# Optimization experiments

Measured on AMD Instinct MI355X. Metric: run time of the kernel, lower is better.

Reference implementation:

```python
import jax, jax.numpy as jnp
import numpy as np

TIMESTEPS = 1000

def _cosine_schedule(T, s=0.008):
    # Nichol & Dhariwal cosine schedule
    x = np.linspace(0.0, T, T + 1, dtype=np.float64)
    acp = np.cos(((x / T) + s) / (1.0 + s) * np.pi / 2.0) ** 2
    acp = acp / acp[0]
    betas = np.clip(1.0 - acp[1:] / acp[:-1], 1e-4, 0.999)
    alphas_cumprod = np.cumprod(1.0 - betas)
    return (betas.astype(np.float32),
            np.sqrt(alphas_cumprod).astype(np.float32),
            np.sqrt(1.0 - alphas_cumprod).astype(np.float32))

BETAS, SQRT_ACP, SQRT_OM_ACP = _cosine_schedule(TIMESTEPS)

B = 2048            # crystals
N_PER = 64          # atoms per crystal (uniform ragged groups)
N = B * N_PER       # total atoms
NODE_DIM = 64
N_SPECIES = 100

def setup_inputs() -> dict:
    key = jax.random.key(0)
    ks = jax.random.split(key, 10)
    frac_coords = jax.random.uniform(ks[0], (N, 3), dtype=jnp.float32)
    noise = jax.random.normal(ks[1], (N, 3), dtype=jnp.float32)
    pred_noise = jax.random.normal(ks[2], (N, 3), dtype=jnp.float32)
    h_final = jax.random.normal(ks[3], (N, NODE_DIM), dtype=jnp.float32)
    # lattice: identity-dominated cells ~5 Angstrom with small perturbation
    lattice = 5.0 * jnp.eye(3, dtype=jnp.float32)[None] + 0.2 * jax.random.normal(ks[4], (B, 3, 3), dtype=jnp.float32)
    W1 = jax.random.normal(ks[5], (NODE_DIM, 128), dtype=jnp.float32) * (1.0 / np.sqrt(NODE_DIM))
    b1 = jnp.zeros((128,), dtype=jnp.float32)
    W2 = jax.random.normal(ks[6], (128, N_SPECIES), dtype=jnp.float32) * (1.0 / np.sqrt(128.0))
    b2 = jnp.zeros((N_SPECIES,), dtype=jnp.float32)
    t = jax.random.randint(ks[7], (B,), 0, TIMESTEPS)
    batch_indices = jnp.repeat(jnp.arange(B), N_PER)
    species = jax.random.randint(ks[8], (N,), 0, N_SPECIES)
    return {"frac_coords": frac_coords, "noise": noise, "pred_noise": pred_noise,
            "h_final": h_final, "lattice": lattice, "W1": W1, "b1": b1,
            "W2": W2, "b2": b2, "t": t, "batch_indices": batch_indices,
            "species": species}

def reference(frac_coords, noise, pred_noise, h_final, lattice, W1, b1, W2, b2,
              t, batch_indices, species):
    sqrt_acp = jnp.asarray(SQRT_ACP)
    sqrt_om = jnp.asarray(SQRT_OM_ACP)
    t_nodes = t[batch_indices]                       # [N]
    sa = sqrt_acp[t_nodes][:, None]                  # [N,1]
    so = sqrt_om[t_nodes][:, None]                   # [N,1]
    # q_sample + periodic wrap
    x_t = sa * frac_coords + so * noise
    x_t = x_t - jnp.floor(x_t)
    # diffusion MSE (dynamics output pred_noise supplied as input)
    loss_diffusion = jnp.mean((pred_noise - noise) ** 2)
    # predicted x0, wrapped
    pred_x0 = (x_t - so * pred_noise) / sa
    pred_x0 = pred_x0 - jnp.floor(pred_x0)
    # vectorized ragged PBC repulsion (uniform groups of N_PER atoms)
    bsz = lattice.shape[0]
    n = frac_coords.shape[0] // bsz
    f = pred_x0.reshape(bsz, n, 3)                   # [B,n,3]
    diff = f[:, :, None, :] - f[:, None, :, :]       # [B,n,n,3]
    diff = diff - jnp.round(diff)                    # minimum-image convention
    diff_c = jnp.einsum('bijk,bkl->bijl', diff, lattice)
    dist_sq = jnp.sum(diff_c ** 2, axis=-1)          # [B,n,n]
    eye = jnp.eye(n, dtype=bool)
    dist_sq = jnp.where(eye[None], 1e10, dist_sq)    # fill_diagonal_(inf)
    dist = jnp.sqrt(dist_sq + 1e-8)
    rep = jax.nn.relu(0.8 - dist) ** 2
    l_repulsion = jnp.sum(rep) / n / bsz
    loss_diffusion = loss_diffusion + 5.0 * l_repulsion
    # species head: Linear -> SiLU -> Linear, cross entropy
    hidden = jax.nn.silu(h_final @ W1 + b1)
    logits = hidden @ W2 + b2                        # [N,100]
    logp = jax.nn.log_softmax(logits, axis=-1)
    loss_species = -jnp.mean(jnp.take_along_axis(logp, species[:, None], axis=-1))
    return (loss_diffusion, loss_species, l_repulsion)
```

## Files before the change

kernel.cpp:

```cpp
#include <hip/hip_runtime.h>
#include <math.h>

#define TSTEPS   1000
#define NB       2048
#define NB2      1024
#define NPER     64
#define NATOMS   (NB*NPER)
#define NDIM     64
#define NHID     128
#define NSPEC    100

typedef __attribute__((ext_vector_type(8))) short bf16x8;
typedef __attribute__((ext_vector_type(4))) float f32x4;

__device__ inline short f2bf(float x) {
  unsigned u = __builtin_bit_cast(unsigned, x);
  u += 0x7fffu + ((u >> 16) & 1u);
  return (short)(u >> 16);
}

__global__ __launch_bounds__(256) void k_sched(float* __restrict__ sacp,
                                               float* __restrict__ som,
                                               const float* __restrict__ W1,
                                               const float* __restrict__ W2,
                                               const float* __restrict__ b2,
                                               unsigned short* __restrict__ w1f,
                                               unsigned short* __restrict__ w2f,
                                               float* __restrict__ b2p) {
  const int tid = threadIdx.x, blk = blockIdx.x;
  if (blk == 0) {
    if (tid < 112) b2p[tid] = (tid < NSPEC) ? b2[tid] : 0.0f;
    __shared__ double sh[256];
    const double PI = 3.14159265358979323846, s = 0.008;
    const int t0 = tid * 4;
    double lg[4], loc = 0.0;
    if (t0 < TSTEPS) {
      double c[5];
      #pragma unroll
      for (int i = 0; i < 5; ++i) {
        double u = (((double)(t0 + i) / (double)TSTEPS) + s) / (1.0 + s) * PI * 0.5;
        c[i] = cos(u);
      }
      #pragma unroll
      for (int i = 0; i < 4; ++i) {
        double beta = 1.0 - (c[i+1]*c[i+1]) / (c[i]*c[i]);
        beta = fmin(fmax(beta, 1e-4), 0.999);
        lg[i] = log(1.0 - beta);
        loc += lg[i];
      }
    }
    sh[tid] = loc;
    __syncthreads();
    for (int off = 1; off < 256; off <<= 1) {
      double add = (tid >= off) ? sh[tid - off] : 0.0;
      __syncthreads();
      sh[tid] += add;
      __syncthreads();
    }
    if (t0 < TSTEPS) {
      double run = sh[tid] - loc;
      #pragma unroll
      for (int i = 0; i < 4; ++i) {
        run += lg[i];
        double cum = exp(run);
        sacp[t0+i] = (float)sqrt(cum);
        som[t0+i]  = (float)sqrt(1.0 - cum);
      }
    }
  } else if (blk <= 4) {
    const int c0 = (blk - 1) * 256 + tid;
    const int lane = c0 & 63, t = c0 >> 6;
    const int kk = t & 1, nt = t >> 1;
    const int q = lane >> 4, l15 = lane & 15;
    __attribute__((aligned(16))) unsigned short v[8];
    #pragma unroll
    for (int j = 0; j < 8; ++j) {
      int k = kk*32 + q*8 + j;
      v[j] = (unsigned short)f2bf(W1[k*NHID + nt*16 + l15]);
    }
    *(uint4*)(w1f + (size_t)c0*8) = *(const uint4*)v;
  } else {
    for (int c0 = (blk - 5) * 256 + tid; c0 < 3584; c0 += 1792) {
      const int lane = c0 & 63, t = c0 >> 6;
      const int kk = t & 3, nt = t >> 2;
      const int q = lane >> 4, l15 = lane & 15;
      const int cls = nt*16 + l15;
      __attribute__((aligned(16))) unsigned short v[8];
      #pragma unroll
      for (int j = 0; j < 8; ++j) {
        int k = kk*32 + q*8 + j;
        v[j] = (cls < NSPEC) ? (unsigned short)f2bf(W2[k*NSPEC + cls]) : 0;
      }
      *(uint4*)(w2f + (size_t)c0*8) = *(const uint4*)v;
    }
  }
}

__global__ __launch_bounds__(256) void k_main(const float* __restrict__ hfin,
                                              const float* __restrict__ b1,
                                              const float* __restrict__ b2p,
                                              const int*   __restrict__ spec,
                                              const unsigned short* __restrict__ w1f,
                                              const unsigned short* __restrict__ w2f,
                                              const float* __restrict__ frac,
                                              const float* __restrict__ noise,
                                              const float* __restrict__ pnoise,
                                              const float* __restrict__ lattice,
                                              const int*   __restrict__ tarr,
                                              const float* __restrict__ sacp,
                                              const float* __restrict__ som,
                                              float* __restrict__ mseP,
                                              float* __restrict__ repP,
                                              float* __restrict__ specP) {
  __shared__ __attribute__((aligned(16))) unsigned short Hs[4*4096];
  const int tid  = threadIdx.x;
  const int wave = tid >> 6, lane = tid & 63;
  const int q = lane >> 4, l15 = lane & 15;
  const int b = blockIdx.x;
  const int atomBase = b * 128;
  unsigned short* HsW = Hs + wave*4096;

  const int cu = __builtin_amdgcn_readfirstlane(2*b + (wave >> 1));
  const int tt = tarr[cu];
  const float sa = sacp[tt], so = som[tt];
  const float rsa = __builtin_amdgcn_rcpf(sa);
  float px0, px1, px2, msep;
  {
    const size_t a = (size_t)cu*64 + lane;
    const float3 fr = *(const float3*)(frac   + 3*a);
    const float3 nz = *(const float3*)(noise  + 3*a);
    const float3 pn = *(const float3*)(pnoise + 3*a);
    float xt0 = fmaf(so, nz.x, sa*fr.x); xt0 -= floorf(xt0);
    float xt1 = fmaf(so, nz.y, sa*fr.y); xt1 -= floorf(xt1);
    float xt2 = fmaf(so, nz.z, sa*fr.z); xt2 -= floorf(xt2);
    px0 = (xt0 - so*pn.x)*rsa; px0 -= floorf(px0);
    px1 = (xt1 - so*pn.y)*rsa; px1 -= floorf(px1);
    px2 = (xt2 - so*pn.z)*rsa; px2 -= floorf(px2);
    float d0 = pn.x - nz.x, d1 = pn.y - nz.y, d2 = pn.z - nz.z;
    msep = fmaf(d0, d0, fmaf(d1, d1, d2*d2));
  }

  bf16x8 aF[2][2];
  #pragma unroll
  for (int at = 0; at < 2; ++at) {
    const float* rp = hfin + (size_t)(atomBase + wave*32 + at*16 + l15) * NDIM;
    #pragma unroll
    for (int kk = 0; kk < 2; ++kk) {
      const float4 p = *(const float4*)(rp + kk*32 + q*8);
      const float4 r = *(const float4*)(rp + kk*32 + q*8 + 4);
      bf16x8 a;
      a[0]=f2bf(p.x); a[1]=f2bf(p.y); a[2]=f2bf(p.z); a[3]=f2bf(p.w);
      a[4]=f2bf(r.x); a[5]=f2bf(r.y); a[6]=f2bf(r.z); a[7]=f2bf(r.w);
      aF[at][kk] = a;
    }
  }

  #pragma unroll
  for (int nt = 0; nt < 8; ++nt) {
    f32x4 dA = (f32x4){0.f,0.f,0.f,0.f}, dB = dA;
    #pragma unroll
    for (int kk = 0; kk < 2; ++kk) {
      bf16x8 wt = *(const bf16x8*)(w1f + (size_t)(((nt*2 + kk)*64 + lane))*8);
      dA = __builtin_amdgcn_mfma_f32_16x16x32_bf16(wt, aF[0][kk], dA, 0, 0, 0);
      dB = __builtin_amdgcn_mfma_f32_16x16x32_bf16(wt, aF[1][kk], dB, 0, 0, 0);
    }
    const float4 bv = *(const float4*)(b1 + nt*16 + q*4);
    #pragma unroll
    for (int at = 0; at < 2; ++at) {
      const f32x4 d = at ? dB : dA;
      float sl[4];
      #pragma unroll
      for (int r = 0; r < 4; ++r) {
        float x = d[r] + ((const float*)&bv)[r];
        float e = __expf(-x);
        sl[r] = x * __builtin_amdgcn_rcpf(1.0f + e);
      }
      uint2 pk;
      pk.x = ((unsigned)(unsigned short)f2bf(sl[0])) | (((unsigned)(unsigned short)f2bf(sl[1])) << 16);
      pk.y = ((unsigned)(unsigned short)f2bf(sl[2])) | (((unsigned)(unsigned short)f2bf(sl[3])) << 16);
      *(uint2*)(HsW + at*2048 + (nt*2 + (q>>1))*128 + l15*8 + (q&1)*4) = pk;
    }
  }
  __builtin_amdgcn_wave_barrier();

  bf16x8 a2[2][4];
  #pragma unroll
  for (int at = 0; at < 2; ++at)
    #pragma unroll
    for (int kk = 0; kk < 4; ++kk)
      a2[at][kk] = *(const bf16x8*)(HsW + at*2048 + (kk*4 + q)*128 + l15*8);

  const int tgtA = spec[atomBase + wave*32 + l15];
  const int tgtB = spec[atomBase + wave*32 + 16 + l15];
  float mA = -1e30f, sA = 0.0f, ltA = 0.0f;
  float mB = -1e30f, sB = 0.0f, ltB = 0.0f;
  #pragma unroll
  for (int nt = 0; nt < 7; ++nt) {
    f32x4 dA = (f32x4){0.f,0.f,0.f,0.f}, dB = dA;
    #pragma unroll
    for (int kk = 0; kk < 4; ++kk) {
      bf16x8 wt = *(const bf16x8*)(w2f + (size_t)(((nt*4 + kk)*64 + lane))*8);
      dA = __builtin_amdgcn_mfma_f32_16x16x32_bf16(wt, a2[0][kk], dA, 0, 0, 0);
      dB = __builtin_amdgcn_mfma_f32_16x16x32_bf16(wt, a2[1][kk], dB, 0, 0, 0);
    }
    const float4 bb = *(const float4*)(b2p + nt*16 + q*4);
    float vA[4], vB[4], vmA = -1e30f, vmB = -1e30f;
    #pragma unroll
    for (int r = 0; r < 4; ++r) {
      const int cls = nt*16 + q*4 + r;
      float xa = dA[r] + ((const float*)&bb)[r];
      float xb = dB[r] + ((const float*)&bb)[r];
      xa = (cls < NSPEC) ? xa : -1e30f;
      xb = (cls < NSPEC) ? xb : -1e30f;
      ltA += (cls == tgtA) ? xa : 0.0f;
      ltB += (cls == tgtB) ? xb : 0.0f;
      vA[r] = xa; vB[r] = xb;
      vmA = fmaxf(vmA, xa); vmB = fmaxf(vmB, xb);
    }
    float mnA = fmaxf(mA, vmA), mnB = fmaxf(mB, vmB);
    sA = sA*__expf(mA - mnA) + __expf(vA[0]-mnA) + __expf(vA[1]-mnA)
                             + __expf(vA[2]-mnA) + __expf(vA[3]-mnA);
    sB = sB*__expf(mB - mnB) + __expf(vB[0]-mnB) + __expf(vB[1]-mnB)
                             + __expf(vB[2]-mnB) + __expf(vB[3]-mnB);
    mA = mnA; mB = mnB;
  }
  #pragma unroll
  for (int d = 16; d <= 32; d <<= 1) {
    float omA = __shfl_xor(mA, d, 64), osA = __shfl_xor(sA, d, 64);
    float omB = __shfl_xor(mB, d, 64), osB = __shfl_xor(sB, d, 64);
    float mnA = fmaxf(mA, omA), mnB = fmaxf(mB, omB);
    sA = sA*__expf(mA - mnA) + osA*__expf(omA - mnA);
    sB = sB*__expf(mB - mnB) + osB*__expf(omB - mnB);
    mA = mnA; mB = mnB;
    ltA += __shfl_xor(ltA, d, 64);
    ltB += __shfl_xor(ltB, d, 64);
  }
  float logp = (ltA - mA - __logf(sA)) + (ltB - mB - __logf(sB));
  #pragma unroll
  for (int d = 1; d < 16; d <<= 1) logp += __shfl_xor(logp, d, 64);

  const float* L = lattice + cu*9;
  const float L00=L[0],L01=L[1],L02=L[2],
              L10=L[3],L11=L[4],L12=L[5],
              L20=L[6],L21=L[7],L22=L[8];
  const int ibase = (wave & 1) * 32;
  float rep = 0.0f;
  #pragma unroll 8
  for (int it = 0; it < 32; ++it) {
    const int i = ibase + it;
    float xi = __shfl(px0, i, 64);
    float yi = __shfl(px1, i, 64);
    float zi = __shfl(px2, i, 64);
    if (i != lane) {
      float dx = xi - px0; dx -= rintf(dx);
      float dy = yi - px1; dy -= rintf(dy);
      float dz = zi - px2; dz -= rintf(dz);
      float cx = dx*L00 + dy*L10 + dz*L20;
      float cy = dx*L01 + dy*L11 + dz*L21;
      float cz = dx*L02 + dy*L12 + dz*L22;
      float d2 = fmaf(cx, cx, fmaf(cy, cy, cz*cz)) + 1e-8f;
      float r  = 0.8f - __builtin_amdgcn_sqrtf(d2);
      if (r > 0.0f) rep = fmaf(r, r, rep);
    }
  }
  #pragma unroll
  for (int o = 32; o > 0; o >>= 1) {
    rep  += __shfl_down(rep,  o, 64);
    msep += __shfl_down(msep, o, 64);
  }
  if (lane == 0) {
    specP[b*4 + wave] = logp;
    repP [b*4 + wave] = rep;
    if ((wave & 1) == 0) mseP[b*2 + (wave>>1)] = msep;
  }
}

__global__ __launch_bounds__(1024) void k_fin(const float* __restrict__ mseP,
                                              const float* __restrict__ repP,
                                              const float* __restrict__ specP,
                                              float* __restrict__ out) {
  __shared__ double sh[48];
  const int tid = threadIdx.x;
  double m = 0.0, r = 0.0, s = 0.0;
  for (int i = tid; i < NB2*4; i += 1024) {
    r += (double)repP[i];
    s += (double)specP[i];
    if (i < NB2*2) m += (double)mseP[i];
  }
  #pragma unroll
  for (int o = 32; o > 0; o >>= 1) {
    m += __shfl_down(m, o, 64);
    r += __shfl_down(r, o, 64);
    s += __shfl_down(s, o, 64);
  }
  const int w = tid >> 6, lane = tid & 63;
  if (lane == 0) { sh[w] = m; sh[16+w] = r; sh[32+w] = s; }
  __syncthreads();
  if (tid == 0) {
    double M=0, R=0, S=0;
    for (int i = 0; i < 16; ++i) { M += sh[i]; R += sh[16+i]; S += sh[32+i]; }
    double mse   = M / (double)(NATOMS*3);
    double lrep  = R / (double)NATOMS;
    double lspec = -S / (double)NATOMS;
    out[0] = (float)(mse + 5.0*lrep);
    out[1] = (float)lspec;
    out[2] = (float)lrep;
  }
}

extern "C" void kernel_launch(void* const* d_in, const int* in_sizes, int n_in,
                              void* d_out, int out_size, void* d_ws, size_t ws_size,
                              hipStream_t stream) {
  const float* frac    = (const float*)d_in[0];
  const float* noise   = (const float*)d_in[1];
  const float* pnoise  = (const float*)d_in[2];
  const float* hfin    = (const float*)d_in[3];
  const float* lattice = (const float*)d_in[4];
  const float* W1      = (const float*)d_in[5];
  const float* b1      = (const float*)d_in[6];
  const float* W2      = (const float*)d_in[7];
  const float* b2      = (const float*)d_in[8];
  const int*   tarr    = (const int*)d_in[9];
  const int*   spec    = (const int*)d_in[11];
  float* out = (float*)d_out;

  float*  sacp = (float*)d_ws;
  float*  som  = sacp + 1024;
  unsigned short* w1f = (unsigned short*)((char*)d_ws + 8192);
  unsigned short* w2f = (unsigned short*)((char*)d_ws + 24576);
  float* b2p   = (float*)((char*)d_ws + 53248);
  float* mseP  = (float*)((char*)d_ws + 53760);
  float* repP  = (float*)((char*)d_ws + 61952);
  float* specP = (float*)((char*)d_ws + 78336);

  k_sched<<<dim3(12),  dim3(256),  0, stream>>>(sacp, som, W1, W2, b2, w1f, w2f, b2p);
  k_main <<<dim3(NB2), dim3(256),  0, stream>>>(hfin, b1, b2p, spec, w1f, w2f,
                                                frac, noise, pnoise, lattice,
                                                tarr, sacp, som, mseP, repP, specP);
  k_fin  <<<dim3(1),   dim3(1024), 0, stream>>>(mseP, repP, specP, out);
}
```

Before: 127.3 us.

## Exploit pair symmetry in repulsion, drop softmax max tracking, truncate bf16 packing

The pairwise repulsion loop now uses the symmetry of the distance. Each lane handles circular offsets 1..32 split across the two waves of a crystal, and the offset-32 pair is weighted so it is not double counted. This halves the sqrt and distance work and removes the diagonal branch. The log-softmax drops the online max rescaling and sums exp(logit) directly, which assumes logits stay small enough not to overflow. Float-to-bf16 conversion switches from round-to-nearest to truncation packed two per word, cutting ALU work at some cost in accuracy.

```diff
diff --git a/kernel.cpp b/kernel.cpp
--- a/kernel.cpp
+++ b/kernel.cpp
@@ -17,6 +17,11 @@
   unsigned u = __builtin_bit_cast(unsigned, x);
   u += 0x7fffu + ((u >> 16) & 1u);
   return (short)(u >> 16);
+}
+
+__device__ inline unsigned pk_trunc(float lo, float hi) {
+  return (__builtin_bit_cast(unsigned, hi) & 0xffff0000u) |
+         (__builtin_bit_cast(unsigned, lo) >> 16);
 }
 
 __global__ __launch_bounds__(256) void k_sched(float* __restrict__ sacp,
@@ -139,6 +144,8 @@
     float d0 = pn.x - nz.x, d1 = pn.y - nz.y, d2 = pn.z - nz.z;
     msep = fmaf(d0, d0, fmaf(d1, d1, d2*d2));
   }
+  const int tgtA = spec[atomBase + wave*32 + l15];
+  const int tgtB = spec[atomBase + wave*32 + 16 + l15];
 
   bf16x8 aF[2][2];
   #pragma unroll
@@ -148,10 +155,10 @@
     for (int kk = 0; kk < 2; ++kk) {
       const float4 p = *(const float4*)(rp + kk*32 + q*8);
       const float4 r = *(const float4*)(rp + kk*32 + q*8 + 4);
-      bf16x8 a;
-      a[0]=f2bf(p.x); a[1]=f2bf(p.y); a[2]=f2bf(p.z); a[3]=f2bf(p.w);
-      a[4]=f2bf(r.x); a[5]=f2bf(r.y); a[6]=f2bf(r.z); a[7]=f2bf(r.w);
-      aF[at][kk] = a;
+      uint4 w;
+      w.x = pk_trunc(p.x, p.y); w.y = pk_trunc(p.z, p.w);
+      w.z = pk_trunc(r.x, r.y); w.w = pk_trunc(r.z, r.w);
+      aF[at][kk] = __builtin_bit_cast(bf16x8, w);
     }
   }
 
@@ -176,8 +183,8 @@
         sl[r] = x * __builtin_amdgcn_rcpf(1.0f + e);
       }
       uint2 pk;
-      pk.x = ((unsigned)(unsigned short)f2bf(sl[0])) | (((unsigned)(unsigned short)f2bf(sl[1])) << 16);
-      pk.y = ((unsigned)(unsigned short)f2bf(sl[2])) | (((unsigned)(unsigned short)f2bf(sl[3])) << 16);
+      pk.x = pk_trunc(sl[0], sl[1]);
+      pk.y = pk_trunc(sl[2], sl[3]);
       *(uint2*)(HsW + at*2048 + (nt*2 + (q>>1))*128 + l15*8 + (q&1)*4) = pk;
     }
   }
@@ -190,10 +197,7 @@
     for (int kk = 0; kk < 4; ++kk)
       a2[at][kk] = *(const bf16x8*)(HsW + at*2048 + (kk*4 + q)*128 + l15*8);
 
-  const int tgtA = spec[atomBase + wave*32 + l15];
-  const int tgtB = spec[atomBase + wave*32 + 16 + l15];
-  float mA = -1e30f, sA = 0.0f, ltA = 0.0f;
-  float mB = -1e30f, sB = 0.0f, ltB = 0.0f;
+  float sA = 0.0f, sB = 0.0f, ltA = 0.0f, ltB = 0.0f;
   #pragma unroll
   for (int nt = 0; nt < 7; ++nt) {
     f32x4 dA = (f32x4){0.f,0.f,0.f,0.f}, dB = dA;
@@ -204,38 +208,23 @@
       dB = __builtin_amdgcn_mfma_f32_16x16x32_bf16(wt, a2[1][kk], dB, 0, 0, 0);
     }
     const float4 bb = *(const float4*)(b2p + nt*16 + q*4);
-    float vA[4], vB[4], vmA = -1e30f, vmB = -1e30f;
     #pragma unroll
     for (int r = 0; r < 4; ++r) {
       const int cls = nt*16 + q*4 + r;
       float xa = dA[r] + ((const float*)&bb)[r];
       float xb = dB[r] + ((const float*)&bb)[r];
-      xa = (cls < NSPEC) ? xa : -1e30f;
-      xb = (cls < NSPEC) ? xb : -1e30f;
+      float ea = (cls < NSPEC) ? __expf(xa) : 0.0f;
+      float eb = (cls < NSPEC) ? __expf(xb) : 0.0f;
+      sA += ea; sB += eb;
       ltA += (cls == tgtA) ? xa : 0.0f;
       ltB += (cls == tgtB) ? xb : 0.0f;
-      vA[r] = xa; vB[r] = xb;
-      vmA = fmaxf(vmA, xa); vmB = fmaxf(vmB, xb);
-    }
-    float mnA = fmaxf(mA, vmA), mnB = fmaxf(mB, vmB);
-    sA = sA*__expf(mA - mnA) + __expf(vA[0]-mnA) + __expf(vA[1]-mnA)
-                             + __expf(vA[2]-mnA) + __expf(vA[3]-mnA);
-    sB = sB*__expf(mB - mnB) + __expf(vB[0]-mnB) + __expf(vB[1]-mnB)
-                             + __expf(vB[2]-mnB) + __expf(vB[3]-mnB);
-    mA = mnA; mB = mnB;
-  }
-  #pragma unroll
-  for (int d = 16; d <= 32; d <<= 1) {
-    float omA = __shfl_xor(mA, d, 64), osA = __shfl_xor(sA, d, 64);
-    float omB = __shfl_xor(mB, d, 64), osB = __shfl_xor(sB, d, 64);
-    float mnA = fmaxf(mA, omA), mnB = fmaxf(mB, omB);
-    sA = sA*__expf(mA - mnA) + osA*__expf(omA - mnA);
-    sB = sB*__expf(mB - mnB) + osB*__expf(omB - mnB);
-    mA = mnA; mB = mnB;
-    ltA += __shfl_xor(ltA, d, 64);
-    ltB += __shfl_xor(ltB, d, 64);
-  }
-  float logp = (ltA - mA - __logf(sA)) + (ltB - mB - __logf(sB));
+    }
+  }
+  sA  += __shfl_xor(sA, 16, 64);  sA  += __shfl_xor(sA, 32, 64);
+  sB  += __shfl_xor(sB, 16, 64);  sB  += __shfl_xor(sB, 32, 64);
+  ltA += __shfl_xor(ltA, 16, 64); ltA += __shfl_xor(ltA, 32, 64);
+  ltB += __shfl_xor(ltB, 16, 64); ltB += __shfl_xor(ltB, 32, 64);
+  float logp = (ltA - __logf(sA)) + (ltB - __logf(sB));
   #pragma unroll
   for (int d = 1; d < 16; d <<= 1) logp += __shfl_xor(logp, d, 64);
 
@@ -243,26 +232,28 @@
   const float L00=L[0],L01=L[1],L02=L[2],
               L10=L[3],L11=L[4],L12=L[5],
               L20=L[6],L21=L[7],L22=L[8];
-  const int ibase = (wave & 1) * 32;
-  float rep = 0.0f;
-  #pragma unroll 8
-  for (int it = 0; it < 32; ++it) {
-    const int i = ibase + it;
-    float xi = __shfl(px0, i, 64);
-    float yi = __shfl(px1, i, 64);
-    float zi = __shfl(px2, i, 64);
-    if (i != lane) {
-      float dx = xi - px0; dx -= rintf(dx);
-      float dy = yi - px1; dy -= rintf(dy);
-      float dz = zi - px2; dz -= rintf(dz);
-      float cx = dx*L00 + dy*L10 + dz*L20;
-      float cy = dx*L01 + dy*L11 + dz*L21;
-      float cz = dx*L02 + dy*L12 + dz*L22;
-      float d2 = fmaf(cx, cx, fmaf(cy, cy, cz*cz)) + 1e-8f;
-      float r  = 0.8f - __builtin_amdgcn_sqrtf(d2);
-      if (r > 0.0f) rep = fmaf(r, r, rep);
-    }
-  }
+  const int sBase = (wave & 1) ? 17 : 1;
+  float rep2 = 0.0f, repLast = 0.0f;
+  #pragma unroll
+  for (int it = 0; it < 16; ++it) {
+    const int s = sBase + it;
+    const int src = (lane + s) & 63;
+    float xj = __shfl(px0, src, 64);
+    float yj = __shfl(px1, src, 64);
+    float zj = __shfl(px2, src, 64);
+    float dx = px0 - xj; dx -= rintf(dx);
+    float dy = px1 - yj; dy -= rintf(dy);
+    float dz = px2 - zj; dz -= rintf(dz);
+    float cx = dx*L00 + dy*L10 + dz*L20;
+    float cy = dx*L01 + dy*L11 + dz*L21;
+    float cz = dx*L02 + dy*L12 + dz*L22;
+    float d2 = fmaf(cx, cx, fmaf(cy, cy, cz*cz)) + 1e-8f;
+    float r  = fmaxf(0.8f - __builtin_amdgcn_sqrtf(d2), 0.0f);
+    float rr = r * r;
+    if (it < 15) rep2 += rr; else repLast = rr;
+  }
+  const float wLast = (wave & 1) ? 1.0f : 2.0f;
+  float rep = fmaf(2.0f, rep2, wLast * repLast);
   #pragma unroll
   for (int o = 32; o > 0; o >>= 1) {
     rep  += __shfl_down(rep,  o, 64);
```

Measured after the change: 123.7 us. -2.9%, faster.
